# Performance work log

Hardware: AMD Instinct MI355X
Metric: run time of the kernel (lower is better)

Reference implementation:

```python
import jax, jax.numpy as jnp
import numpy as np

N_NODES = 50000
N_EDGES = 800000
IN_DIM = 100

def setup_inputs() -> dict:
    key = jax.random.key(0)
    ks = jax.random.split(key, 12)
    nf = jax.random.normal(ks[0], (3, IN_DIM), dtype=jnp.float32)
    tid = jax.random.randint(ks[1], (N_NODES,), 0, 4)
    xr = jax.random.normal(ks[2], (N_NODES, IN_DIM), dtype=jnp.float32)
    # nodes of type 0/1/2 get exact prototype rows; type 3 ('edge') gets random rows
    x = jnp.where((tid < 3)[:, None], nf[jnp.clip(tid, 0, 2)], xr)
    edge_index = jax.random.randint(ks[3], (2, N_EDGES), 0, N_NODES, dtype=jnp.int32)
    def w(k, fi, fo):
        return jax.random.normal(k, (fi, fo), dtype=jnp.float32) * (1.0 / np.sqrt(fi))
    return {
        'x': x, 'node_feature': nf, 'edge_index': edge_index,
        'W1': w(ks[4], 100, 512), 'b1': jnp.zeros((512,), jnp.float32),
        'W2': w(ks[5], 512, 256), 'b2': jnp.zeros((256,), jnp.float32),
        'W3': w(ks[6], 256, 128), 'b3': jnp.zeros((128,), jnp.float32),
        'W4': w(ks[7], 128, 200), 'b4': jnp.zeros((200,), jnp.float32),
    }

def _gcn_forward(x, edge_index, W1, b1, W2, b2, W3, b3, W4, b4):
    N = x.shape[0]
    loop = jnp.arange(N, dtype=edge_index.dtype)
    src = jnp.concatenate([edge_index[0], loop])
    dst = jnp.concatenate([edge_index[1], loop])
    deg = jax.ops.segment_sum(jnp.ones_like(src, dtype=x.dtype), dst, num_segments=N)
    dinv = jnp.where(deg > 0, jax.lax.rsqrt(deg), 0.0)
    norm = dinv[src] * dinv[dst]  # symmetric GCN normalization with self-loops
    def gcn(h, W, b):
        h = h @ W
        agg = jax.ops.segment_sum(h[src] * norm[:, None], dst, num_segments=N)
        return agg + b
    out = jax.nn.relu(gcn(x, W1, b1))
    out = jax.nn.relu(gcn(out, W2, b2))
    out = jax.nn.relu(gcn(out, W3, b3))
    out = jax.nn.relu(gcn(out, W4, b4))
    return out

def _cat_mean(x, out, node_feature):
    # Vectorized replacement of the per-node python loop: output slot order is
    # init(nf0)->0, accept(nf2)->1, edge(other)->2, common(nf1)->3, matching the
    # original append order when all groups are nonempty.
    eq = jnp.all(x[:, None, :] == node_feature[None, :, :], axis=-1)  # [N,3]
    group = jnp.where(eq[:, 0], 0, jnp.where(eq[:, 1], 3, jnp.where(eq[:, 2], 1, 2)))
    sums = jax.ops.segment_sum(out, group, num_segments=4)            # [4,D]
    cnt = jax.ops.segment_sum(jnp.ones((x.shape[0],), out.dtype), group, num_segments=4)
    means = jnp.where(cnt[:, None] > 0, sums / jnp.maximum(cnt, 1.0)[:, None], 0.0)
    return means.reshape(1, -1)  # [1, 4*D]

def reference(x, node_feature, edge_index, W1, b1, W2, b2, W3, b3, W4, b4):
    out = _gcn_forward(x, edge_index, W1, b1, W2, b2, W3, b3, W4, b4)
    return _cat_mean(x, out, node_feature)
```

## Files before the change

### kernel.cpp

```cpp
#include <hip/hip_runtime.h>
#include <stdint.h>

typedef __attribute__((ext_vector_type(8))) short bf16x8;
typedef __attribute__((ext_vector_type(4))) float f32x4;

__device__ __forceinline__ float bf2f(ushort h) {
    union { uint u; float f; } v; v.u = ((uint)h) << 16; return v.f;
}
__device__ __forceinline__ ushort f2bf(float f) {
    union { float f; uint u; } v; v.f = f;
    uint u = v.u;
    return (ushort)((u + 0x7fffu + ((u >> 16) & 1u)) >> 16);
}

__device__ __forceinline__ void gll(const ushort* g, ushort* l) {
    __builtin_amdgcn_global_load_lds(
        (const __attribute__((address_space(1))) void*)g,
        (__attribute__((address_space(3))) void*)l, 16, 0, 0);
}

template <int VEC>
__device__ __forceinline__ void ldbf(const ushort* p, float* v) {
    if constexpr (VEC == 4) {
        uint2 u = *(const uint2*)p;
        v[0] = bf2f((ushort)(u.x & 0xffffu));
        v[1] = bf2f((ushort)(u.x >> 16));
        v[2] = bf2f((ushort)(u.y & 0xffffu));
        v[3] = bf2f((ushort)(u.y >> 16));
    } else {
        uint4 u = *(const uint4*)p;
        v[0] = bf2f((ushort)(u.x & 0xffffu));
        v[1] = bf2f((ushort)(u.x >> 16));
        v[2] = bf2f((ushort)(u.y & 0xffffu));
        v[3] = bf2f((ushort)(u.y >> 16));
        v[4] = bf2f((ushort)(u.z & 0xffffu));
        v[5] = bf2f((ushort)(u.z >> 16));
        v[6] = bf2f((ushort)(u.w & 0xffffu));
        v[7] = bf2f((ushort)(u.w >> 16));
    }
}


__device__ __forceinline__ void tr2_one(const float* __restrict__ W,
                                        ushort* __restrict__ WTh, ushort* __restrict__ WTl,
                                        int K, int Nc, int KP, int idx) {
    int n = idx / KP, k = idx % KP;
    float w = (n < Nc && k < K) ? W[(size_t)k * Nc + n] : 0.0f;
    ushort hi = f2bf(w);
    ushort lo = f2bf(w - bf2f(hi));
    WTh[idx] = hi;
    WTl[idx] = lo;
}

__global__ void k_init(const uint* __restrict__ xu, const uint* __restrict__ nfu,
                       ushort* __restrict__ xb, int* __restrict__ gid, int NN,
                       const int* __restrict__ dst, int E, int* __restrict__ deg,
                       const float* __restrict__ W1, const float* __restrict__ W2,
                       const float* __restrict__ W3, const float* __restrict__ W4,
                       ushort* __restrict__ WT1h, ushort* __restrict__ WT1l,
                       ushort* __restrict__ WT2h, ushort* __restrict__ WT2l,
                       ushort* __restrict__ WT3h, ushort* __restrict__ WT3l,
                       ushort* __restrict__ WT4h, ushort* __restrict__ WT4l,
                       int PB, int EB) {
    int b = blockIdx.x;
    if (b < PB) {
        int wid = b * 4 + (threadIdx.x >> 6);
        int lane = threadIdx.x & 63;
        if (wid >= NN) return;
        int c0 = lane * 2;
        uint w = 0u;
        int m0 = 1, m1 = 1, m2 = 1;
        if (c0 < 100) {
            uint2 xv = *(const uint2*)&xu[(size_t)wid * 100 + c0];
            uint2 a = *(const uint2*)&nfu[c0];
            uint2 bb = *(const uint2*)&nfu[100 + c0];
            uint2 c = *(const uint2*)&nfu[200 + c0];
            m0 = (xv.x == a.x) & (xv.y == a.y);
            m1 = (xv.x == bb.x) & (xv.y == bb.y);
            m2 = (xv.x == c.x) & (xv.y == c.y);
            w = (uint)f2bf(__uint_as_float(xv.x)) | ((uint)f2bf(__uint_as_float(xv.y)) << 16);
        }
        int e0 = __all(m0), e1 = __all(m1), e2 = __all(m2);
        *(uint*)&xb[(size_t)wid * 128 + c0] = w;
        if (lane == 0) gid[wid] = e0 ? 0 : (e1 ? 3 : (e2 ? 1 : 2));
    } else if (b < PB + EB) {
        int e = (b - PB) * 256 + threadIdx.x;
        if (e < E) atomicAdd(&deg[dst[e]], 1);
    } else {
        int idx = (b - PB - EB) * 256 + threadIdx.x;
        if (idx < 65536) tr2_one(W1, WT1h, WT1l, 100, 512, 128, idx);
        else if (idx < 196608) tr2_one(W2, WT2h, WT2l, 512, 256, 512, idx - 65536);
        else if (idx < 229376) tr2_one(W3, WT3h, WT3l, 256, 128, 256, idx - 196608);
        else if (idx < 262144) tr2_one(W4, WT4h, WT4l, 128, 200, 128, idx - 229376);
    }
}


__global__ void k_scanA(const int* __restrict__ deg, int* __restrict__ offs,
                        int* __restrict__ bsum, float* __restrict__ dinv, int NN) {
    __shared__ int lds[256];
    int t = threadIdx.x;
    int i = blockIdx.x * 256 + t;
    int v = (i < NN) ? deg[i] : 0;
    if (i < NN) dinv[i] = 1.0f / sqrtf((float)(v + 1));
    lds[t] = v;
    __syncthreads();
    for (int d = 1; d < 256; d <<= 1) {
        int u = (t >= d) ? lds[t - d] : 0;
        __syncthreads();
        lds[t] += u;
        __syncthreads();
    }
    if (i < NN) offs[i] = lds[t] - v;
    if (t == 255) bsum[blockIdx.x] = lds[255];
}

__global__ void k_scanB(int* __restrict__ bsum, int nb) {
    __shared__ int lds[256];
    int t = threadIdx.x;
    int v = (t < nb) ? bsum[t] : 0;
    lds[t] = v;
    __syncthreads();
    for (int d = 1; d < 256; d <<= 1) {
        int u = (t >= d) ? lds[t - d] : 0;
        __syncthreads();
        lds[t] += u;
        __syncthreads();
    }
    if (t < nb) bsum[t] = lds[t] - v;
}

__global__ void k_fill(const int* __restrict__ src, const int* __restrict__ dst, int E,
                       const float* __restrict__ dinv, int* __restrict__ offs,
                       const int* __restrict__ bsum,
                       int* __restrict__ cur, uint2* __restrict__ epk, int NN,
                       int* __restrict__ goffs) {
    int i = blockIdx.x * blockDim.x + threadIdx.x;
    if (i < NN) goffs[i] = offs[i] + bsum[i >> 8];
    if (i >= E) return;
    int s = src[i], d = dst[i];
    int p = offs[d] + bsum[d >> 8] + atomicAdd(&cur[d], 1);
    epk[p] = make_uint2((uint)s, __float_as_uint(dinv[s] * dinv[d]));
}


template <int D, bool BR>
__global__ void k_aggs(const ushort* __restrict__ H, ushort* __restrict__ outb,
                       const float* __restrict__ dinv, const int* __restrict__ offs,
                       const int* __restrict__ deg, const uint2* __restrict__ epk,
                       const float* __restrict__ bias, int NN, int NNpad) {
    constexpr int VEC = D / 32;
    int wid = (int)((blockIdx.x * blockDim.x + threadIdx.x) >> 6);
    int lane = threadIdx.x & 63;
    int half = lane >> 5, sl = lane & 31;
    if (wid >= NNpad) return;
    int c0 = sl * VEC;
    ushort* op = outb + (size_t)wid * D + c0;
    if (wid >= NN) {
        if (half == 0) {
            if (VEC == 4) *(uint2*)op = make_uint2(0u, 0u);
            else { uint4 z; z.x = z.y = z.z = z.w = 0u; *(uint4*)op = z; }
        }
        return;
    }
    float acc[VEC];
#pragma unroll
    for (int j = 0; j < VEC; ++j) acc[j] = 0.0f;
    int beg = offs[wid], d = deg[wid];
    if (half == 0) {
        float t0[VEC];
        ldbf<VEC>(H + (size_t)wid * D + c0, t0);
        float di = dinv[wid];
        float sw = di * di;
#pragma unroll
        for (int j = 0; j < VEC; ++j) acc[j] = sw * t0[j];
    }
    int d0 = (d + 1) >> 1;
    int e = beg + half * d0;
    int end = e + (half ? (d - d0) : d0);
    for (; e + 3 < end; e += 4) {
        uint2 q0 = epk[e], q1 = epk[e + 1], q2 = epk[e + 2], q3 = epk[e + 3];
        float t0[VEC], t1[VEC], t2[VEC], t3[VEC];
        ldbf<VEC>(H + (size_t)q0.x * D + c0, t0);
        ldbf<VEC>(H + (size_t)q1.x * D + c0, t1);
        ldbf<VEC>(H + (size_t)q2.x * D + c0, t2);
        ldbf<VEC>(H + (size_t)q3.x * D + c0, t3);
        float w0 = __uint_as_float(q0.y), w1 = __uint_as_float(q1.y);
        float w2 = __uint_as_float(q2.y), w3 = __uint_as_float(q3.y);
#pragma unroll
        for (int j = 0; j < VEC; ++j) acc[j] += w0 * t0[j];
#pragma unroll
        for (int j = 0; j < VEC; ++j) acc[j] += w1 * t1[j];
#pragma unroll
        for (int j = 0; j < VEC; ++j) acc[j] += w2 * t2[j];
#pragma unroll
        for (int j = 0; j < VEC; ++j) acc[j] += w3 * t3[j];
    }
    for (; e < end; ++e) {
        uint2 q0 = epk[e];
        float t0[VEC];
        ldbf<VEC>(H + (size_t)q0.x * D + c0, t0);
        float w0 = __uint_as_float(q0.y);
#pragma unroll
        for (int j = 0; j < VEC; ++j) acc[j] += w0 * t0[j];
    }
#pragma unroll
    for (int j = 0; j < VEC; ++j) acc[j] += __shfl_xor(acc[j], 32);
    if (half == 0) {
        ushort r[VEC];
#pragma unroll
        for (int j = 0; j < VEC; ++j) {
            float v = acc[j];
            if (BR) v = fmaxf(v + bias[c0 + j], 0.0f);
            r[j] = f2bf(v);
        }
        if (VEC == 4) {
            uint2 w;
            w.x = (uint)r[0] | ((uint)r[1] << 16);
            w.y = (uint)r[2] | ((uint)r[3] << 16);
            *(uint2*)op = w;
        } else {
            uint4 w;
            w.x = (uint)r[0] | ((uint)r[1] << 16);
            w.y = (uint)r[2] | ((uint)r[3] << 16);
            w.z = (uint)r[4] | ((uint)r[5] << 16);
            w.w = (uint)r[6] | ((uint)r[7] << 16);
            *(uint4*)op = w;
        }
    }
}


template <bool BR, int OUT>
__global__ __launch_bounds__(256) void k_gemm(
        const ushort* __restrict__ A,
        const ushort* __restrict__ Bh, const ushort* __restrict__ Bl,
        const float* __restrict__ bias,
        ushort* __restrict__ Cb,
        int Nc, int K, int tNb,
        const int* __restrict__ gid, float* __restrict__ gsum, int NN) {
    __shared__ union {
        ushort st[3][128 * 32];
        float epi[64 * 132];
    } sm;
    __shared__ int gcode[64];
    int bm = blockIdx.x / tNb, bn = blockIdx.x % tNb;
    int m0 = bm * 128, n0 = bn * 128;
    int wv = threadIdx.x >> 6, lane = threadIdx.x & 63;
    int l15 = lane & 15, quad = lane >> 4;
    const ushort* gsrc;
    ushort* ldst;
    int ng;
    if (wv == 0)      { gsrc = A  + (size_t)m0 * K;        ldst = sm.st[0];        ng = 4; }
    else if (wv == 1) { gsrc = A  + (size_t)(m0 + 64) * K; ldst = sm.st[0] + 2048; ng = 4; }
    else if (wv == 2) { gsrc = Bh + (size_t)n0 * K;        ldst = sm.st[1];        ng = 8; }
    else              { gsrc = Bl + (size_t)n0 * K;        ldst = sm.st[2];        ng = 8; }
    const ushort* gBase = gsrc + (size_t)(lane >> 2) * K + (lane & 3) * 8;
    int wm = (wv >> 1) * 64, wn = (wv & 1) * 64;
    const ushort* sA_ = sm.st[0];
    const ushort* sBh_ = sm.st[1];
    const ushort* sBl_ = sm.st[2];
    f32x4 acc[4][4] = {};
    for (int k0 = 0; k0 < K; k0 += 32) {
        for (int i = 0; i < ng; ++i)
            gll(gBase + (size_t)(16 * i) * K + k0, ldst + i * 512);
        __syncthreads();
        bf16x8 Af[4], Bfh[4], Bfl[4];
#pragma unroll
        for (int i = 0; i < 4; ++i) {
            int ra = (wm + 16 * i + l15) * 32 + quad * 8;
            int rb = (wn + 16 * i + l15) * 32 + quad * 8;
            Af[i]  = *(const bf16x8*)(sA_ + ra);
            Bfh[i] = *(const bf16x8*)(sBh_ + rb);
            Bfl[i] = *(const bf16x8*)(sBl_ + rb);
        }
#pragma unroll
        for (int mi = 0; mi < 4; ++mi)
#pragma unroll
            for (int ni = 0; ni < 4; ++ni) {
                acc[mi][ni] = __builtin_amdgcn_mfma_f32_16x16x32_bf16(Af[mi], Bfh[ni], acc[mi][ni], 0, 0, 0);
                acc[mi][ni] = __builtin_amdgcn_mfma_f32_16x16x32_bf16(Af[mi], Bfl[ni], acc[mi][ni], 0, 0, 0);
            }
        __syncthreads();
    }
    float bia[4] = {0.f, 0.f, 0.f, 0.f};
    if (BR) {
#pragma unroll
        for (int ni = 0; ni < 4; ++ni) {
            int col = n0 + wn + 16 * ni + l15;
            if (col < Nc) bia[ni] = bias[col];
        }
    }
    float* epi = sm.epi;
    int t = threadIdx.x;
    float s0 = 0.f, s1 = 0.f, s2 = 0.f, s3 = 0.f;
    int colR = t & 127, rg = t >> 7;
    for (int half = 0; half < 2; ++half) {
        if ((wv >> 1) == half) {
#pragma unroll
            for (int mi = 0; mi < 4; ++mi)
#pragma unroll
                for (int r = 0; r < 4; ++r) {
                    int rl = mi * 16 + quad * 4 + r;
#pragma unroll
                    for (int ni = 0; ni < 4; ++ni) {
                        float v = acc[mi][ni][r];
                        if (BR) v = fmaxf(v + bia[ni], 0.0f);
                        epi[rl * 132 + wn + ni * 16 + l15] = v;
                    }
                }
        }
        if (OUT == 2 && t < 64) {
            int grow = m0 + half * 64 + t;
            gcode[t] = (grow < NN) ? gid[grow] : -1;
        }
        __syncthreads();
        if (OUT == 2) {
#pragma unroll 4
            for (int r = 0; r < 32; ++r) {
                int row = rg * 32 + r;
                int g = gcode[row];
                float v = epi[row * 132 + colR];
                s0 += (g == 0) ? v : 0.f;
                s1 += (g == 1) ? v : 0.f;
                s2 += (g == 2) ? v : 0.f;
                s3 += (g == 3) ? v : 0.f;
            }
        } else {
#pragma unroll
            for (int j = 0; j < 16; ++j) {
                int e = (j * 256 + t) * 2;
                int rl = e >> 7, cl = e & 127;
                int grow = m0 + half * 64 + rl;
                int gcol = n0 + cl;
                float v0 = epi[rl * 132 + cl];
                float v1 = epi[rl * 132 + cl + 1];
                *(uint*)&Cb[(size_t)grow * Nc + gcol] = (uint)f2bf(v0) | ((uint)f2bf(v1) << 16);
            }
        }
        __syncthreads();
    }
    if (OUT == 2) {
        if (rg == 1) {
            epi[colR * 4 + 0] = s0; epi[colR * 4 + 1] = s1;
            epi[colR * 4 + 2] = s2; epi[colR * 4 + 3] = s3;
        }
        __syncthreads();
        if (rg == 0) {
            s0 += epi[colR * 4 + 0]; s1 += epi[colR * 4 + 1];
            s2 += epi[colR * 4 + 2]; s3 += epi[colR * 4 + 3];
            int gcol = n0 + colR;
            if (gcol < Nc) {
                atomicAdd(&gsum[0 * Nc + gcol], s0);
                atomicAdd(&gsum[1 * Nc + gcol], s1);
                atomicAdd(&gsum[2 * Nc + gcol], s2);
                atomicAdd(&gsum[3 * Nc + gcol], s3);
            }
        }
    }
}


__global__ void k_final(const float* __restrict__ gsum, const int* __restrict__ gid,
                        int NN, float* __restrict__ out) {
    __shared__ int cnt[4];
    int t = threadIdx.x;
    if (t < 4) cnt[t] = 0;
    __syncthreads();
    int c0 = 0, c1 = 0, c2 = 0, c3 = 0;
    for (int i = t; i < NN; i += 1024) {
        int g = gid[i];
        c0 += (g == 0); c1 += (g == 1); c2 += (g == 2); c3 += (g == 3);
    }
    if (c0) atomicAdd(&cnt[0], c0);
    if (c1) atomicAdd(&cnt[1], c1);
    if (c2) atomicAdd(&cnt[2], c2);
    if (c3) atomicAdd(&cnt[3], c3);
    __syncthreads();
    if (t < 800) {
        int g = t / 200;
        int c = cnt[g];
        out[t] = (c > 0) ? gsum[t] / (float)c : 0.0f;
    }
}


extern "C" void kernel_launch(void* const* d_in, const int* in_sizes, int n_in,
                              void* d_out, int out_size, void* d_ws, size_t ws_size,
                              hipStream_t stream) {
    const float* x  = (const float*)d_in[0];
    const float* nf = (const float*)d_in[1];
    const int* ei   = (const int*)d_in[2];
    const float* W1 = (const float*)d_in[3];
    const float* b1 = (const float*)d_in[4];
    const float* W2 = (const float*)d_in[5];
    const float* b2 = (const float*)d_in[6];
    const float* W3 = (const float*)d_in[7];
    const float* b3 = (const float*)d_in[8];
    const float* W4 = (const float*)d_in[9];
    const float* b4 = (const float*)d_in[10];
    float* out = (float*)d_out;

    const int NN = in_sizes[0] / 100;
    const int E  = in_sizes[2] / 2;
    const int MPAD = ((NN + 127) / 128) * 128;
    const int NB = (NN + 255) / 256;
    const int PB = (NN + 3) / 4;
    const int EB = (E + 255) / 256;
    const int TB = 1024;
    const int* src = ei;
    const int* dst = ei + E;

    char* p = (char*)d_ws;
    auto alloc = [&](size_t bytes) -> char* {
        char* r = p;
        p += (bytes + 255) & ~(size_t)255;
        return r;
    };
    char* zz = p;
    int*   deg  = (int*)alloc((size_t)NN * 4);
    int*   cur  = (int*)alloc((size_t)NN * 4);
    float* gsum = (float*)alloc(800 * 4);
    size_t zz_bytes = (size_t)(p - zz);
    float* dinv = (float*)alloc((size_t)NN * 4);
    int*   offs = (int*)alloc((size_t)NN * 4);
    int*   goffs = (int*)alloc((size_t)NN * 4);
    int*   bsum = (int*)alloc(1024);
    int*   gid  = (int*)alloc((size_t)NN * 4);
    uint2* epk  = (uint2*)alloc((size_t)E * 8);
    ushort* WT1h = (ushort*)alloc((size_t)512 * 128 * 2);
    ushort* WT1l = (ushort*)alloc((size_t)512 * 128 * 2);
    ushort* WT2h = (ushort*)alloc((size_t)256 * 512 * 2);
    ushort* WT2l = (ushort*)alloc((size_t)256 * 512 * 2);
    ushort* WT3h = (ushort*)alloc((size_t)128 * 256 * 2);
    ushort* WT3l = (ushort*)alloc((size_t)128 * 256 * 2);
    ushort* WT4h = (ushort*)alloc((size_t)256 * 128 * 2);
    ushort* WT4l = (ushort*)alloc((size_t)256 * 128 * 2);
    ushort* xb = (ushort*)alloc((size_t)NN * 128 * 2);
    ushort* P1 = (ushort*)alloc((size_t)MPAD * 128 * 2);
    ushort* H1 = (ushort*)alloc((size_t)MPAD * 512 * 2);
    ushort* T2 = (ushort*)alloc((size_t)MPAD * 256 * 2);
    ushort* H2 = (ushort*)alloc((size_t)MPAD * 256 * 2);
    ushort* T3 = (ushort*)alloc((size_t)MPAD * 128 * 2);
    ushort* H3 = (ushort*)alloc((size_t)MPAD * 128 * 2);
    ushort* P4 = (ushort*)alloc((size_t)MPAD * 128 * 2);

    hipMemsetAsync(zz, 0, zz_bytes, stream);

    k_init<<<PB + EB + TB, 256, 0, stream>>>(
        (const uint*)x, (const uint*)nf, xb, gid, NN, dst, E, deg,
        W1, W2, W3, W4, WT1h, WT1l, WT2h, WT2l, WT3h, WT3l, WT4h, WT4l, PB, EB);
    k_scanA<<<NB, 256, 0, stream>>>(deg, offs, bsum, dinv, NN);
    k_scanB<<<1, 256, 0, stream>>>(bsum, NB);
    k_fill<<<EB, 256, 0, stream>>>(src, dst, E, dinv, offs, bsum, cur, epk, NN, goffs);

    int aggBlocks = MPAD / 4;
    int mB = MPAD / 128;

    k_aggs<128, false><<<aggBlocks, 256, 0, stream>>>(xb, P1, dinv, goffs, deg, epk, nullptr, NN, MPAD);
    k_gemm<true, 1><<<mB * 4, 256, 0, stream>>>(P1, WT1h, WT1l, b1, H1, 512, 128, 4, nullptr, nullptr, 0);
    k_gemm<false, 1><<<mB * 2, 256, 0, stream>>>(H1, WT2h, WT2l, nullptr, T2, 256, 512, 2, nullptr, nullptr, 0);
    k_aggs<256, true><<<aggBlocks, 256, 0, stream>>>(T2, H2, dinv, goffs, deg, epk, b2, NN, MPAD);
    k_gemm<false, 1><<<mB * 1, 256, 0, stream>>>(H2, WT3h, WT3l, nullptr, T3, 128, 256, 1, nullptr, nullptr, 0);
    k_aggs<128, true><<<aggBlocks, 256, 0, stream>>>(T3, H3, dinv, goffs, deg, epk, b3, NN, MPAD);
    k_aggs<128, false><<<aggBlocks, 256, 0, stream>>>(H3, P4, dinv, goffs, deg, epk, nullptr, NN, MPAD);
    k_gemm<true, 2><<<mB * 2, 256, 0, stream>>>(P4, WT4h, WT4l, b4, nullptr, 200, 128, 2, gid, gsum, NN);

    k_final<<<1, 1024, 0, stream>>>(gsum, gid, NN, out);
}
```

Baseline: 474.1 us.

## Fold scanB into fill, group counts into scanA, and final into last GEMM

Removes the single-block k_scanB kernel by having every k_fill block redundantly scan the block sums in shared memory. Group counts move into k_scanA through shared and global atomics. The k_final kernel is replaced by a last-block-done pattern in the final GEMM, using a done counter and threadfence. This cuts two kernel launches and a serial single-block pass, at the cost of redundant per-block scans and an extra atomic in each GEMM block.

Result: slower. 487.2 us (+2.8%).

```diff
diff --git a/kernel.cpp b/kernel.cpp
--- a/kernel.cpp
+++ b/kernel.cpp
@@ -97,14 +97,20 @@
 
 
 __global__ void k_scanA(const int* __restrict__ deg, int* __restrict__ offs,
-                        int* __restrict__ bsum, float* __restrict__ dinv, int NN) {
+                        int* __restrict__ bsum, float* __restrict__ dinv,
+                        const int* __restrict__ gid, int* __restrict__ gcnt, int NN) {
     __shared__ int lds[256];
+    __shared__ int cnt4[4];
     int t = threadIdx.x;
+    if (t < 4) cnt4[t] = 0;
     int i = blockIdx.x * 256 + t;
     int v = (i < NN) ? deg[i] : 0;
-    if (i < NN) dinv[i] = 1.0f / sqrtf((float)(v + 1));
+    if (i < NN) {
+        dinv[i] = 1.0f / sqrtf((float)(v + 1));
+    }
     lds[t] = v;
     __syncthreads();
+    if (i < NN) atomicAdd(&cnt4[gid[i]], 1);
     for (int d = 1; d < 256; d <<= 1) {
         int u = (t >= d) ? lds[t - d] : 0;
         __syncthreads();
@@ -113,33 +119,36 @@
     }
     if (i < NN) offs[i] = lds[t] - v;
     if (t == 255) bsum[blockIdx.x] = lds[255];
-}
-
-__global__ void k_scanB(int* __restrict__ bsum, int nb) {
-    __shared__ int lds[256];
+    __syncthreads();
+    if (t < 4 && cnt4[t]) atomicAdd(&gcnt[t], cnt4[t]);
+}
+
+
+__global__ void k_fill(const int* __restrict__ src, const int* __restrict__ dst, int E,
+                       const float* __restrict__ dinv, const int* __restrict__ offs,
+                       const int* __restrict__ bsum,
+                       int* __restrict__ cur, uint2* __restrict__ epk, int NN, int NB,
+                       int* __restrict__ goffs) {
+    __shared__ int sex[256];
     int t = threadIdx.x;
-    int v = (t < nb) ? bsum[t] : 0;
-    lds[t] = v;
+    int v = (t < NB) ? bsum[t] : 0;
+    sex[t] = v;
     __syncthreads();
     for (int d = 1; d < 256; d <<= 1) {
-        int u = (t >= d) ? lds[t - d] : 0;
-        __syncthreads();
-        lds[t] += u;
-        __syncthreads();
-    }
-    if (t < nb) bsum[t] = lds[t] - v;
-}
-
-__global__ void k_fill(const int* __restrict__ src, const int* __restrict__ dst, int E,
-                       const float* __restrict__ dinv, int* __restrict__ offs,
-                       const int* __restrict__ bsum,
-                       int* __restrict__ cur, uint2* __restrict__ epk, int NN,
-                       int* __restrict__ goffs) {
-    int i = blockIdx.x * blockDim.x + threadIdx.x;
-    if (i < NN) goffs[i] = offs[i] + bsum[i >> 8];
+        int u = (t >= d) ? sex[t - d] : 0;
+        __syncthreads();
+        sex[t] += u;
+        __syncthreads();
+    }
+    int incl = sex[t];
+    __syncthreads();
+    sex[t] = incl - v;
+    __syncthreads();
+    int i = blockIdx.x * 256 + t;
+    if (i < NN) goffs[i] = offs[i] + sex[i >> 8];
     if (i >= E) return;
     int s = src[i], d = dst[i];
-    int p = offs[d] + bsum[d >> 8] + atomicAdd(&cur[d], 1);
+    int p = offs[d] + sex[d >> 8] + atomicAdd(&cur[d], 1);
     epk[p] = make_uint2((uint)s, __float_as_uint(dinv[s] * dinv[d]));
 }
 
@@ -238,12 +247,14 @@
         const float* __restrict__ bias,
         ushort* __restrict__ Cb,
         int Nc, int K, int tNb,
-        const int* __restrict__ gid, float* __restrict__ gsum, int NN) {
+        const int* __restrict__ gid, float* __restrict__ gsum, int NN,
+        int* __restrict__ gcnt, float* __restrict__ outF, int* __restrict__ donecnt) {
     __shared__ union {
         ushort st[3][128 * 32];
         float epi[64 * 132];
     } sm;
     __shared__ int gcode[64];
+    __shared__ int lastFlag;
     int bm = blockIdx.x / tNb, bn = blockIdx.x % tNb;
     int m0 = bm * 128, n0 = bn * 128;
     int wv = threadIdx.x >> 6, lane = threadIdx.x & 63;
@@ -357,30 +368,19 @@
                 atomicAdd(&gsum[3 * Nc + gcol], s3);
             }
         }
-    }
-}
-
-
-__global__ void k_final(const float* __restrict__ gsum, const int* __restrict__ gid,
-                        int NN, float* __restrict__ out) {
-    __shared__ int cnt[4];
-    int t = threadIdx.x;
-    if (t < 4) cnt[t] = 0;
-    __syncthreads();
-    int c0 = 0, c1 = 0, c2 = 0, c3 = 0;
-    for (int i = t; i < NN; i += 1024) {
-        int g = gid[i];
-        c0 += (g == 0); c1 += (g == 1); c2 += (g == 2); c3 += (g == 3);
-    }
-    if (c0) atomicAdd(&cnt[0], c0);
-    if (c1) atomicAdd(&cnt[1], c1);
-    if (c2) atomicAdd(&cnt[2], c2);
-    if (c3) atomicAdd(&cnt[3], c3);
-    __syncthreads();
-    if (t < 800) {
-        int g = t / 200;
-        int c = cnt[g];
-        out[t] = (c > 0) ? gsum[t] / (float)c : 0.0f;
+        __threadfence();
+        __syncthreads();
+        if (t == 0) lastFlag = (atomicAdd(donecnt, 1) == (int)gridDim.x - 1);
+        __syncthreads();
+        if (lastFlag) {
+            __threadfence();
+            for (int j = t; j < 800; j += 256) {
+                int g = j / 200, col = j % 200;
+                int c = atomicAdd(&gcnt[g], 0);
+                float s = atomicAdd(&gsum[(size_t)g * Nc + col], 0.0f);
+                outF[j] = (c > 0) ? s / (float)c : 0.0f;
+            }
+        }
     }
 }
 
@@ -421,7 +421,9 @@
     int*   deg  = (int*)alloc((size_t)NN * 4);
     int*   cur  = (int*)alloc((size_t)NN * 4);
     float* gsum = (float*)alloc(800 * 4);
+    int*   gcnt = (int*)alloc(256);
     size_t zz_bytes = (size_t)(p - zz);
+    int*   donecnt = gcnt + 4;
     float* dinv = (float*)alloc((size_t)NN * 4);
     int*   offs = (int*)alloc((size_t)NN * 4);
     int*   goffs = (int*)alloc((size_t)NN * 4);
@@ -450,21 +452,18 @@
     k_init<<<PB + EB + TB, 256, 0, stream>>>(
         (const uint*)x, (const uint*)nf, xb, gid, NN, dst, E, deg,
         W1, W2, W3, W4, WT1h, WT1l, WT2h, WT2l, WT3h, WT3l, WT4h, WT4l, PB, EB);
-    k_scanA<<<NB, 256, 0, stream>>>(deg, offs, bsum, dinv, NN);
-    k_scanB<<<1, 256, 0, stream>>>(bsum, NB);
-    k_fill<<<EB, 256, 0, stream>>>(src, dst, E, dinv, offs, bsum, cur, epk, NN, goffs);
+    k_scanA<<<NB, 256, 0, stream>>>(deg, offs, bsum, dinv, gid, gcnt, NN);
+    k_fill<<<EB, 256, 0, stream>>>(src, dst, E, dinv, offs, bsum, cur, epk, NN, NB, goffs);
 
     int aggBlocks = MPAD / 4;
     int mB = MPAD / 128;
 
     k_aggs<128, false><<<aggBlocks, 256, 0, stream>>>(xb, P1, dinv, goffs, deg, epk, nullptr, NN, MPAD);
-    k_gemm<true, 1><<<mB * 4, 256, 0, stream>>>(P1, WT1h, WT1l, b1, H1, 512, 128, 4, nullptr, nullptr, 0);
-    k_gemm<false, 1><<<mB * 2, 256, 0, stream>>>(H1, WT2h, WT2l, nullptr, T2, 256, 512, 2, nullptr, nullptr, 0);
+    k_gemm<true, 1><<<mB * 4, 256, 0, stream>>>(P1, WT1h, WT1l, b1, H1, 512, 128, 4, nullptr, nullptr, 0, nullptr, nullptr, nullptr);
+    k_gemm<false, 1><<<mB * 2, 256, 0, stream>>>(H1, WT2h, WT2l, nullptr, T2, 256, 512, 2, nullptr, nullptr, 0, nullptr, nullptr, nullptr);
     k_aggs<256, true><<<aggBlocks, 256, 0, stream>>>(T2, H2, dinv, goffs, deg, epk, b2, NN, MPAD);
-    k_gemm<false, 1><<<mB * 1, 256, 0, stream>>>(H2, WT3h, WT3l, nullptr, T3, 128, 256, 1, nullptr, nullptr, 0);
+    k_gemm<false, 1><<<mB * 1, 256, 0, stream>>>(H2, WT3h, WT3l, nullptr, T3, 128, 256, 1, nullptr, nullptr, 0, nullptr, nullptr, nullptr);
     k_aggs<128, true><<<aggBlocks, 256, 0, stream>>>(T3, H3, dinv, goffs, deg, epk, b3, NN, MPAD);
     k_aggs<128, false><<<aggBlocks, 256, 0, stream>>>(H3, P4, dinv, goffs, deg, epk, nullptr, NN, MPAD);
-    k_gemm<true, 2><<<mB * 2, 256, 0, stream>>>(P4, WT4h, WT4l, b4, nullptr, 200, 128, 2, gid, gsum, NN);
-
-    k_final<<<1, 1024, 0, stream>>>(gsum, gid, NN, out);
-}
+    k_gemm<true, 2><<<mB * 2, 256, 0, stream>>>(P4, WT4h, WT4l, b4, nullptr, 200, 128, 2, gid, gsum, NN, gcnt, out, donecnt);
+}
```
